# Performance work log

Measured on AMD Instinct MI355X. Metric: run time of the kernel, lower is better.

The kernel has to match this reference:

```python
import jax, jax.numpy as jnp
import numpy as np


def setup_inputs() -> dict:
    key = jax.random.key(0)
    ks = jax.random.split(key, 8)
    dim, E = 128, 8
    b, t, h, w = 2, 16, 64, 64
    scale = 1.0 / np.sqrt(dim)
    return {
        "x": jax.random.normal(ks[0], (b, dim, t, h, w), jnp.float32),
        "gate_w": jax.random.normal(ks[1], (dim, E), jnp.float32) * scale,
        "gate_b": jax.random.normal(ks[2], (E,), jnp.float32) * 0.01,
        "W1": jax.random.normal(ks[3], (E, dim, dim), jnp.float32) * scale,
        "b1": jax.random.normal(ks[4], (E, dim), jnp.float32) * 0.01,
        "alpha": jnp.full((E,), 0.25, jnp.float32),  # PReLU default init
        "W2": jax.random.normal(ks[5], (E, dim, dim), jnp.float32) * scale,
        "b2": jax.random.normal(ks[6], (E, dim), jnp.float32) * 0.01,
        "top_k": 2,
    }


def reference(x, gate_w, gate_b, W1, b1, alpha, W2, b2, top_k):
    b, c, t, h, w = x.shape
    E = gate_w.shape[1]
    # tokens: [N, c] with N = b*t*h*w (matches permute(0,2,3,4,1).reshape(-1,c))
    xf = jnp.transpose(x, (0, 2, 3, 4, 1)).reshape(-1, c)
    N = xf.shape[0]
    logits = xf @ gate_w + gate_b                      # [N, E]
    vals, idx = jax.lax.top_k(logits, top_k)           # [N, K]
    probs = jax.nn.softmax(vals, axis=1)               # softmax over selected logits
    # scatter combine weights to dense [N, E] (zero for unselected experts)
    combine = jnp.zeros((N, E), xf.dtype).at[jnp.arange(N)[:, None], idx].add(probs)
    # expert MLP (1x1x1 conv == per-token linear), scalar PReLU per expert
    h1 = jnp.einsum('nc,eoc->eno', xf, W1) + b1[:, None, :]          # [E, N, c]
    h1 = jnp.maximum(h1, 0) + alpha[:, None, None] * jnp.minimum(h1, 0)
    h2 = jnp.einsum('eno,epo->enp', h1, W2) + b2[:, None, :]         # [E, N, c]
    out = jnp.einsum('ne,enc->nc', combine, h2)                      # weighted combine
    out = jnp.transpose(out.reshape(b, t, h, w, c), (0, 4, 1, 2, 3))
    return out + x
```

## Files before the change

### kernel.cpp

```cpp
#include <hip/hip_runtime.h>

typedef float f32x4 __attribute__((ext_vector_type(4)));
typedef __bf16 bf16x8 __attribute__((ext_vector_type(8)));

#define SPAT 65536
#define CH   128
#define NE   8

#define XS_OFF   0
#define WA_OFF   65536
#define WB_OFF   98304
#define PL_OFF   65536
#define SEL_OFF  131072
#define Q_OFF    132096
#define CB_OFF   134144
#define B1_OFF   138240
#define B2T_OFF  142336
#define AL_OFF   144384
#define LDS_BYTES 144416

static __device__ __forceinline__ unsigned short f2b(float f) {
    unsigned u = __builtin_bit_cast(unsigned, f);
    unsigned r = u + 0x7FFFu + ((u >> 16) & 1u);
    return (unsigned short)(r >> 16);
}
static __device__ __forceinline__ unsigned pk2(float a, float b) {
    return (unsigned)f2b(a) | ((unsigned)f2b(b) << 16);
}

typedef const __attribute__((address_space(1))) void* as1cp;
typedef __attribute__((address_space(3))) void* as3p;
static __device__ __forceinline__ void gload16(const void* g, void* l) {
    __builtin_amdgcn_global_load_lds((as1cp)g, (as3p)l, 16, 0, 0);
}

__global__ void conv_w(const float* __restrict__ W1, const float* __restrict__ W2,
                       unsigned char* __restrict__ wimg) {
    const int gid = blockIdx.x * 256 + threadIdx.x;
    const int mat = gid >> 14;
    const int e   = (gid >> 11) & 7;
    const int o   = (gid >> 4) & 127;
    const int g   = gid & 15;
    const float* s = (mat ? W2 : W1) + (e * 16384 + o * 128 + g * 8);
    uint4 p;
    p.x = pk2(s[0], s[1]); p.y = pk2(s[2], s[3]);
    p.z = pk2(s[4], s[5]); p.w = pk2(s[6], s[7]);
    *(uint4*)(wimg + mat * 262144 + e * 32768 + o * 256 + ((g ^ (o & 7)) * 16)) = p;
}

__global__ __launch_bounds__(1024) __attribute__((amdgpu_waves_per_eu(4, 4)))
void moe_main(const float* __restrict__ x,  const float* __restrict__ gw,
              const float* __restrict__ gb, const float* __restrict__ b1,
              const float* __restrict__ alpha, const float* __restrict__ b2,
              const unsigned char* __restrict__ wimg, float* __restrict__ out)
{
    __shared__ __align__(16) unsigned char smem[LDS_BYTES];
    const int t = threadIdx.x, lane = t & 63, w = t >> 6, blk = blockIdx.x;
    const size_t xbase = (size_t)(blk >> 8) * (size_t)(CH * SPAT) + (size_t)((blk & 255) << 8);

    if (t < 256) ((f32x4*)(smem + B1_OFF))[t] = ((const f32x4*)b1)[t];
    else if (t >= 256 && t < 384) {
        const int j = t - 256;
        uint4 p;
        p.x = pk2(b2[0 * 128 + j], b2[1 * 128 + j]);
        p.y = pk2(b2[2 * 128 + j], b2[3 * 128 + j]);
        p.z = pk2(b2[4 * 128 + j], b2[5 * 128 + j]);
        p.w = pk2(b2[6 * 128 + j], b2[7 * 128 + j]);
        *(uint4*)(smem + B2T_OFF + j * 16) = p;
    } else if (t >= 384 && t < 392) {
        ((float*)(smem + AL_OFF))[t - 384] = alpha[t - 384];
    }

    {
        const int m = t & 255, p = t >> 8;
        f32x4 plo = {0.f,0.f,0.f,0.f}, phi = {0.f,0.f,0.f,0.f};
        #pragma unroll
        for (int cc = 0; cc < 4; ++cc) {
            const int c0 = p * 32 + cc * 8;
            float v[8];
            #pragma unroll
            for (int j = 0; j < 8; ++j) v[j] = x[xbase + (size_t)(c0 + j) * SPAT + m];
            #pragma unroll
            for (int j = 0; j < 8; ++j) {
                const f32x4 g0 = *(const f32x4*)(gw + (c0 + j) * NE);
                const f32x4 g1 = *(const f32x4*)(gw + (c0 + j) * NE + 4);
                plo += v[j] * g0; phi += v[j] * g1;
            }
            uint4 pkv;
            pkv.x = pk2(v[0], v[1]); pkv.y = pk2(v[2], v[3]);
            pkv.z = pk2(v[4], v[5]); pkv.w = pk2(v[6], v[7]);
            const int g = p * 4 + cc;
            *(uint4*)(smem + XS_OFF + m * 256 + ((g ^ (m & 7)) * 16)) = pkv;
        }
        float* pl = (float*)(smem + PL_OFF);
        #pragma unroll
        for (int e2 = 0; e2 < 4; ++e2) {
            pl[(p * 8 + e2)     * 256 + m] = plo[e2];
            pl[(p * 8 + 4 + e2) * 256 + m] = phi[e2];
        }
    }
    __syncthreads();
    if (t < 256) {
        const int m = t;
        const float* pl = (const float*)(smem + PL_OFF);
        float lg[8];
        #pragma unroll
        for (int e2 = 0; e2 < 8; ++e2) lg[e2] = gb[e2];
        #pragma unroll
        for (int pp = 0; pp < 4; ++pp)
            #pragma unroll
            for (int e2 = 0; e2 < 8; ++e2) lg[e2] += pl[(pp * 8 + e2) * 256 + m];
        int i0 = 0; float v0 = lg[0];
        #pragma unroll
        for (int e2 = 1; e2 < 8; ++e2) if (lg[e2] > v0) { v0 = lg[e2]; i0 = e2; }
        int i1 = -1; float v1 = -3.4e38f;
        #pragma unroll
        for (int e2 = 0; e2 < 8; ++e2) if (e2 != i0 && lg[e2] > v1) { v1 = lg[e2]; i1 = e2; }
        const float d  = expf(v1 - v0);
        const float q0 = 1.f / (1.f + d);
        const float q1 = d   / (1.f + d);
        ((unsigned*)(smem + SEL_OFF))[m] = (unsigned)i0 | ((unsigned)i1 << 8);
        ((float*)(smem + Q_OFF))[m * 2]     = q0;
        ((float*)(smem + Q_OFF))[m * 2 + 1] = q1;
        float cb[8];
        #pragma unroll
        for (int e2 = 0; e2 < 8; ++e2) cb[e2] = (e2 == i0) ? q0 : ((e2 == i1) ? q1 : 0.f);
        uint4 cw;
        cw.x = pk2(cb[0], cb[1]); cw.y = pk2(cb[2], cb[3]);
        cw.z = pk2(cb[4], cb[5]); cw.w = pk2(cb[6], cb[7]);
        *(uint4*)(smem + CB_OFF + m * 16) = cw;
    }
    __syncthreads();

    {
        const int goff = w * 1024 + lane * 16, loff = w * 1024;
        #pragma unroll
        for (int r = 0; r < 2; ++r) {
            gload16(wimg + r * 16384 + goff,          smem + WA_OFF + r * 16384 + loff);
            gload16(wimg + 262144 + r * 16384 + goff, smem + WB_OFF + r * 16384 + loff);
        }
    }

    const int mg = w >> 3, ng = w & 7, col = lane & 15, kq = lane >> 4;

    int sel[2]; float cp0[2], cp1[2];
    #pragma unroll
    for (int nf = 0; nf < 2; ++nf) {
        const int tk = ng * 32 + nf * 16 + col;
        sel[nf] = ((const unsigned*)(smem + SEL_OFF))[tk];
        cp0[nf] = ((const float*)(smem + Q_OFF))[tk * 2];
        cp1[nf] = ((const float*)(smem + Q_OFF))[tk * 2 + 1];
    }
    uint4 xb[2][4];
    #pragma unroll
    for (int nf = 0; nf < 2; ++nf) {
        const int row = ng * 32 + nf * 16 + col;
        #pragma unroll
        for (int kt = 0; kt < 4; ++kt)
            xb[nf][kt] = *(const uint4*)(smem + XS_OFF + row * 256 + (((kt * 4 + kq) ^ (row & 7)) * 16));
    }
    __syncthreads();

    f32x4 acc[2][4] = {};

    for (int e = 0; e < NE; ++e) {
        const float alph = ((const float*)(smem + AL_OFF))[e];
        #pragma unroll
        for (int ml = 0; ml < 4; ++ml) {
            const int o = mg * 64 + ml * 16 + col;
            uint4 a1[4];
            #pragma unroll
            for (int kt = 0; kt < 4; ++kt)
                a1[kt] = *(const uint4*)(smem + WA_OFF + o * 256 + (((kt * 4 + kq) ^ (o & 7)) * 16));
            f32x4 h[2] = {};
            #pragma unroll
            for (int kt = 0; kt < 4; ++kt)
                #pragma unroll
                for (int nf = 0; nf < 2; ++nf)
                    h[nf] = __builtin_amdgcn_mfma_f32_16x16x32_bf16(
                        __builtin_bit_cast(bf16x8, a1[kt]),
                        __builtin_bit_cast(bf16x8, xb[nf][kt]), h[nf], 0, 0, 0);
            const int o0 = mg * 64 + ml * 16 + kq * 4;
            const f32x4 b1v = *(const f32x4*)(smem + B1_OFF + e * 512 + o0 * 4);
            #pragma unroll
            for (int nf = 0; nf < 2; ++nf) {
                const float ce = ((sel[nf] & 255) == e) ? cp0[nf]
                               : ((((sel[nf] >> 8) & 255) == e) ? cp1[nf] : 0.f);
                float hv[4];
                #pragma unroll
                for (int i = 0; i < 4; ++i) {
                    float z = h[nf][i] + b1v[i];
                    z = (z > 0.f) ? z : alph * z;
                    hv[i] = z * ce;
                }
                const int tok = ng * 32 + nf * 16 + col;
                const int g   = o0 >> 3;
                uint2 pw; pw.x = pk2(hv[0], hv[1]); pw.y = pk2(hv[2], hv[3]);
                *(uint2*)(smem + XS_OFF + tok * 256 + ((g ^ (tok & 7)) * 16) + ((o0 & 4) << 1)) = pw;
            }
        }
        __syncthreads();
        if (e < 7) {
            const int goff = w * 1024 + lane * 16, loff = w * 1024;
            const unsigned char* src = wimg + (e + 1) * 32768;
            #pragma unroll
            for (int r = 0; r < 2; ++r)
                gload16(src + r * 16384 + goff, smem + WA_OFF + r * 16384 + loff);
        }
        #pragma unroll
        for (int kt = 0; kt < 4; ++kt) {
            uint4 hb[2], wf[4];
            #pragma unroll
            for (int m2 = 0; m2 < 2; ++m2) {
                const int tok = ng * 32 + m2 * 16 + col;
                hb[m2] = *(const uint4*)(smem + XS_OFF + tok * 256 + (((kt * 4 + kq) ^ (tok & 7)) * 16));
            }
            #pragma unroll
            for (int n2 = 0; n2 < 4; ++n2) {
                const int o2 = mg * 64 + n2 * 16 + col;
                wf[n2] = *(const uint4*)(smem + WB_OFF + o2 * 256 + (((kt * 4 + kq) ^ (o2 & 7)) * 16));
            }
            #pragma unroll
            for (int m2 = 0; m2 < 2; ++m2)
                #pragma unroll
                for (int n2 = 0; n2 < 4; ++n2)
                    acc[m2][n2] = __builtin_amdgcn_mfma_f32_16x16x32_bf16(
                        __builtin_bit_cast(bf16x8, hb[m2]),
                        __builtin_bit_cast(bf16x8, wf[n2]), acc[m2][n2], 0, 0, 0);
        }
        __syncthreads();
        if (e < 7) {
            const int goff = w * 1024 + lane * 16, loff = w * 1024;
            const unsigned char* src = wimg + 262144 + (e + 1) * 32768;
            #pragma unroll
            for (int r = 0; r < 2; ++r)
                gload16(src + r * 16384 + goff, smem + WB_OFF + r * 16384 + loff);
        }
    }

    {
        const uint4 z4 = {0u, 0u, 0u, 0u};
        uint4 paf[2], pbf[4];
        #pragma unroll
        for (int m2 = 0; m2 < 2; ++m2) {
            const int tok = ng * 32 + m2 * 16 + col;
            paf[m2] = (kq == 0) ? *(const uint4*)(smem + CB_OFF + tok * 16) : z4;
        }
        #pragma unroll
        for (int n2 = 0; n2 < 4; ++n2) {
            const int o2 = mg * 64 + n2 * 16 + col;
            pbf[n2] = (kq == 0) ? *(const uint4*)(smem + B2T_OFF + o2 * 16) : z4;
        }
        #pragma unroll
        for (int m2 = 0; m2 < 2; ++m2)
            #pragma unroll
            for (int n2 = 0; n2 < 4; ++n2)
                acc[m2][n2] = __builtin_amdgcn_mfma_f32_16x16x32_bf16(
                    __builtin_bit_cast(bf16x8, paf[m2]),
                    __builtin_bit_cast(bf16x8, pbf[n2]), acc[m2][n2], 0, 0, 0);
    }

    #pragma unroll
    for (int m2 = 0; m2 < 2; ++m2) {
        const int tok0 = ng * 32 + m2 * 16 + kq * 4;
        #pragma unroll
        for (int n2 = 0; n2 < 4; ++n2) {
            const int o2 = mg * 64 + n2 * 16 + col;
            const size_t a = xbase + (size_t)o2 * SPAT + tok0;
            const f32x4 xv = *(const f32x4*)(x + a);
            f32x4 r = acc[m2][n2];
            r += xv;
            *(f32x4*)(out + a) = r;
        }
    }
}

extern "C" void kernel_launch(void* const* d_in, const int* in_sizes, int n_in,
                              void* d_out, int out_size, void* d_ws, size_t ws_size,
                              hipStream_t stream) {
    const float* x  = (const float*)d_in[0];
    const float* gw = (const float*)d_in[1];
    const float* gb = (const float*)d_in[2];
    const float* W1 = (const float*)d_in[3];
    const float* b1 = (const float*)d_in[4];
    const float* al = (const float*)d_in[5];
    const float* W2 = (const float*)d_in[6];
    const float* b2 = (const float*)d_in[7];
    (void)in_sizes; (void)n_in; (void)out_size; (void)ws_size;
    unsigned char* wimg = (unsigned char*)d_ws;
    float* out = (float*)d_out;

    conv_w<<<dim3(128), dim3(256), 0, stream>>>(W1, W2, wimg);
    moe_main<<<dim3(512), dim3(1024), 0, stream>>>(x, gw, gb, b1, al, b2, wimg, out);
}
```

Before: 145.0 us.

## Keep expert hidden activations in registers and double-buffer expert weights in LDS

Each wave now owns 16 tokens across all 128 output channels, not a 64x32 tile. The first GEMM's output is packed directly into MFMA A-operand registers for the second GEMM, which works because the W1 rows are permuted at conversion so the accumulator layout matches the needed K ordering. This removes the LDS write/read round trip of the hidden activations. Expert weights now sit in four 32KB LDS slots and are prefetched two experts ahead, replacing the single-buffered reload after each barrier. In exchange, each wave reads the full weight matrices from LDS, increasing LDS read traffic per wave, and register pressure goes up.

```diff
diff --git a/kernel.cpp b/kernel.cpp
--- a/kernel.cpp
+++ b/kernel.cpp
@@ -7,9 +7,8 @@
 #define CH   128
 #define NE   8
 
+#define SLOT(i)  ((i) * 32768)
 #define XS_OFF   0
-#define WA_OFF   65536
-#define WB_OFF   98304
 #define PL_OFF   65536
 #define SEL_OFF  131072
 #define Q_OFF    132096
@@ -41,11 +40,21 @@
     const int e   = (gid >> 11) & 7;
     const int o   = (gid >> 4) & 127;
     const int g   = gid & 15;
-    const float* s = (mat ? W2 : W1) + (e * 16384 + o * 128 + g * 8);
+    int src_row = o;
+    if (mat == 0)
+        src_row = ((o >> 5) << 5) + (((o >> 2) & 3) << 3) + (((o >> 4) & 1) << 2) + (o & 3);
+    const float* s = (mat ? W2 : W1) + (e * 16384 + src_row * 128 + g * 8);
     uint4 p;
     p.x = pk2(s[0], s[1]); p.y = pk2(s[2], s[3]);
     p.z = pk2(s[4], s[5]); p.w = pk2(s[6], s[7]);
     *(uint4*)(wimg + mat * 262144 + e * 32768 + o * 256 + ((g ^ (o & 7)) * 16)) = p;
+}
+
+static __device__ __forceinline__ void stage_w(const unsigned char* __restrict__ src,
+                                               unsigned char* dst, int t) {
+    const int off = t * 16;
+    gload16(src + off,         dst + off);
+    gload16(src + 16384 + off, dst + 16384 + off);
 }
 
 __global__ __launch_bounds__(1024) __attribute__((amdgpu_waves_per_eu(4, 4)))
@@ -57,6 +66,8 @@
     __shared__ __align__(16) unsigned char smem[LDS_BYTES];
     const int t = threadIdx.x, lane = t & 63, w = t >> 6, blk = blockIdx.x;
     const size_t xbase = (size_t)(blk >> 8) * (size_t)(CH * SPAT) + (size_t)((blk & 255) << 8);
+
+    stage_w(wimg, smem + SLOT(3), t);
 
     if (t < 256) ((f32x4*)(smem + B1_OFF))[t] = ((const f32x4*)b1)[t];
     else if (t >= 256 && t < 384) {
@@ -132,146 +143,99 @@
     }
     __syncthreads();
 
-    {
-        const int goff = w * 1024 + lane * 16, loff = w * 1024;
-        #pragma unroll
-        for (int r = 0; r < 2; ++r) {
-            gload16(wimg + r * 16384 + goff,          smem + WA_OFF + r * 16384 + loff);
-            gload16(wimg + 262144 + r * 16384 + goff, smem + WB_OFF + r * 16384 + loff);
-        }
-    }
-
-    const int mg = w >> 3, ng = w & 7, col = lane & 15, kq = lane >> 4;
-
-    int sel[2]; float cp0[2], cp1[2];
+    const int col = lane & 15, kq = lane >> 4;
+    const int tokA = w * 16 + col;
+    const unsigned selu = ((const unsigned*)(smem + SEL_OFF))[tokA];
+    const float cq0 = ((const float*)(smem + Q_OFF))[tokA * 2];
+    const float cq1 = ((const float*)(smem + Q_OFF))[tokA * 2 + 1];
+
+    uint4 xb[4];
     #pragma unroll
-    for (int nf = 0; nf < 2; ++nf) {
-        const int tk = ng * 32 + nf * 16 + col;
-        sel[nf] = ((const unsigned*)(smem + SEL_OFF))[tk];
-        cp0[nf] = ((const float*)(smem + Q_OFF))[tk * 2];
-        cp1[nf] = ((const float*)(smem + Q_OFF))[tk * 2 + 1];
-    }
-    uint4 xb[2][4];
-    #pragma unroll
-    for (int nf = 0; nf < 2; ++nf) {
-        const int row = ng * 32 + nf * 16 + col;
-        #pragma unroll
-        for (int kt = 0; kt < 4; ++kt)
-            xb[nf][kt] = *(const uint4*)(smem + XS_OFF + row * 256 + (((kt * 4 + kq) ^ (row & 7)) * 16));
-    }
+    for (int kt = 0; kt < 4; ++kt)
+        xb[kt] = *(const uint4*)(smem + XS_OFF + tokA * 256 + (((kt * 4 + kq) ^ (tokA & 7)) * 16));
     __syncthreads();
 
-    f32x4 acc[2][4] = {};
-
+    stage_w(wimg + 262144,         smem + SLOT(0), t);
+    stage_w(wimg + 32768,          smem + SLOT(1), t);
+    stage_w(wimg + 262144 + 32768, smem + SLOT(2), t);
+
+    f32x4 acc[8] = {};
+
+    #pragma unroll 1
     for (int e = 0; e < NE; ++e) {
+        const unsigned waOff = 0x18000u ^ ((unsigned)(e & 1) << 16);
+        const unsigned wbOff = ((unsigned)(e & 1) << 16);
+        const unsigned char* WA = smem + waOff;
+        const unsigned char* WB = smem + wbOff;
         const float alph = ((const float*)(smem + AL_OFF))[e];
-        #pragma unroll
-        for (int ml = 0; ml < 4; ++ml) {
-            const int o = mg * 64 + ml * 16 + col;
+        const float ce = ((selu & 255u) == (unsigned)e) ? cq0
+                       : ((((selu >> 8) & 255u) == (unsigned)e) ? cq1 : 0.f);
+
+        uint4 pa[4];
+        #pragma unroll
+        for (int ml = 0; ml < 8; ++ml) {
+            const int o = ml * 16 + col;
             uint4 a1[4];
             #pragma unroll
             for (int kt = 0; kt < 4; ++kt)
-                a1[kt] = *(const uint4*)(smem + WA_OFF + o * 256 + (((kt * 4 + kq) ^ (o & 7)) * 16));
-            f32x4 h[2] = {};
+                a1[kt] = *(const uint4*)(WA + o * 256 + (((kt * 4 + kq) ^ (o & 7)) * 16));
+            f32x4 h = {0.f, 0.f, 0.f, 0.f};
             #pragma unroll
             for (int kt = 0; kt < 4; ++kt)
-                #pragma unroll
-                for (int nf = 0; nf < 2; ++nf)
-                    h[nf] = __builtin_amdgcn_mfma_f32_16x16x32_bf16(
+                h = __builtin_amdgcn_mfma_f32_16x16x32_bf16(
                         __builtin_bit_cast(bf16x8, a1[kt]),
-                        __builtin_bit_cast(bf16x8, xb[nf][kt]), h[nf], 0, 0, 0);
-            const int o0 = mg * 64 + ml * 16 + kq * 4;
-            const f32x4 b1v = *(const f32x4*)(smem + B1_OFF + e * 512 + o0 * 4);
-            #pragma unroll
-            for (int nf = 0; nf < 2; ++nf) {
-                const float ce = ((sel[nf] & 255) == e) ? cp0[nf]
-                               : ((((sel[nf] >> 8) & 255) == e) ? cp1[nf] : 0.f);
-                float hv[4];
-                #pragma unroll
-                for (int i = 0; i < 4; ++i) {
-                    float z = h[nf][i] + b1v[i];
-                    z = (z > 0.f) ? z : alph * z;
-                    hv[i] = z * ce;
-                }
-                const int tok = ng * 32 + nf * 16 + col;
-                const int g   = o0 >> 3;
-                uint2 pw; pw.x = pk2(hv[0], hv[1]); pw.y = pk2(hv[2], hv[3]);
-                *(uint2*)(smem + XS_OFF + tok * 256 + ((g ^ (tok & 7)) * 16) + ((o0 & 4) << 1)) = pw;
+                        __builtin_bit_cast(bf16x8, xb[kt]), h, 0, 0, 0);
+            const int ob = ((ml >> 1) << 5) + (kq << 3) + ((ml & 1) << 2);
+            const f32x4 b1v = *(const f32x4*)(smem + B1_OFF + e * 512 + ob * 4);
+            float hv[4];
+            #pragma unroll
+            for (int i = 0; i < 4; ++i) {
+                float z = h[i] + b1v[i];
+                z = (z > 0.f) ? z : alph * z;
+                hv[i] = z * ce;
             }
+            ((unsigned*)&pa[ml >> 1])[(ml & 1) * 2]     = pk2(hv[0], hv[1]);
+            ((unsigned*)&pa[ml >> 1])[(ml & 1) * 2 + 1] = pk2(hv[2], hv[3]);
         }
         __syncthreads();
-        if (e < 7) {
-            const int goff = w * 1024 + lane * 16, loff = w * 1024;
-            const unsigned char* src = wimg + (e + 1) * 32768;
-            #pragma unroll
-            for (int r = 0; r < 2; ++r)
-                gload16(src + r * 16384 + goff, smem + WA_OFF + r * 16384 + loff);
-        }
+        if (e < 6) stage_w(wimg + (e + 2) * 32768, smem + waOff, t);
+
         #pragma unroll
         for (int kt = 0; kt < 4; ++kt) {
-            uint4 hb[2], wf[4];
-            #pragma unroll
-            for (int m2 = 0; m2 < 2; ++m2) {
-                const int tok = ng * 32 + m2 * 16 + col;
-                hb[m2] = *(const uint4*)(smem + XS_OFF + tok * 256 + (((kt * 4 + kq) ^ (tok & 7)) * 16));
+            #pragma unroll
+            for (int n2 = 0; n2 < 8; ++n2) {
+                const int o2 = n2 * 16 + col;
+                const uint4 wf = *(const uint4*)(WB + o2 * 256 + (((kt * 4 + kq) ^ (o2 & 7)) * 16));
+                acc[n2] = __builtin_amdgcn_mfma_f32_16x16x32_bf16(
+                        __builtin_bit_cast(bf16x8, pa[kt]),
+                        __builtin_bit_cast(bf16x8, wf), acc[n2], 0, 0, 0);
             }
-            #pragma unroll
-            for (int n2 = 0; n2 < 4; ++n2) {
-                const int o2 = mg * 64 + n2 * 16 + col;
-                wf[n2] = *(const uint4*)(smem + WB_OFF + o2 * 256 + (((kt * 4 + kq) ^ (o2 & 7)) * 16));
-            }
-            #pragma unroll
-            for (int m2 = 0; m2 < 2; ++m2)
-                #pragma unroll
-                for (int n2 = 0; n2 < 4; ++n2)
-                    acc[m2][n2] = __builtin_amdgcn_mfma_f32_16x16x32_bf16(
-                        __builtin_bit_cast(bf16x8, hb[m2]),
-                        __builtin_bit_cast(bf16x8, wf[n2]), acc[m2][n2], 0, 0, 0);
         }
         __syncthreads();
-        if (e < 7) {
-            const int goff = w * 1024 + lane * 16, loff = w * 1024;
-            const unsigned char* src = wimg + 262144 + (e + 1) * 32768;
-            #pragma unroll
-            for (int r = 0; r < 2; ++r)
-                gload16(src + r * 16384 + goff, smem + WB_OFF + r * 16384 + loff);
-        }
+        if (e < 6) stage_w(wimg + 262144 + (e + 2) * 32768, smem + wbOff, t);
     }
 
     {
         const uint4 z4 = {0u, 0u, 0u, 0u};
-        uint4 paf[2], pbf[4];
-        #pragma unroll
-        for (int m2 = 0; m2 < 2; ++m2) {
-            const int tok = ng * 32 + m2 * 16 + col;
-            paf[m2] = (kq == 0) ? *(const uint4*)(smem + CB_OFF + tok * 16) : z4;
-        }
-        #pragma unroll
-        for (int n2 = 0; n2 < 4; ++n2) {
-            const int o2 = mg * 64 + n2 * 16 + col;
-            pbf[n2] = (kq == 0) ? *(const uint4*)(smem + B2T_OFF + o2 * 16) : z4;
-        }
-        #pragma unroll
-        for (int m2 = 0; m2 < 2; ++m2)
-            #pragma unroll
-            for (int n2 = 0; n2 < 4; ++n2)
-                acc[m2][n2] = __builtin_amdgcn_mfma_f32_16x16x32_bf16(
-                    __builtin_bit_cast(bf16x8, paf[m2]),
-                    __builtin_bit_cast(bf16x8, pbf[n2]), acc[m2][n2], 0, 0, 0);
-    }
-
+        const uint4 paf = (kq == 0) ? *(const uint4*)(smem + CB_OFF + tokA * 16) : z4;
+        #pragma unroll
+        for (int n2 = 0; n2 < 8; ++n2) {
+            const uint4 pbf = (kq == 0) ? *(const uint4*)(smem + B2T_OFF + (n2 * 16 + col) * 16) : z4;
+            acc[n2] = __builtin_amdgcn_mfma_f32_16x16x32_bf16(
+                    __builtin_bit_cast(bf16x8, paf),
+                    __builtin_bit_cast(bf16x8, pbf), acc[n2], 0, 0, 0);
+        }
+    }
+
+    const int tok0 = w * 16 + kq * 4;
     #pragma unroll
-    for (int m2 = 0; m2 < 2; ++m2) {
-        const int tok0 = ng * 32 + m2 * 16 + kq * 4;
-        #pragma unroll
-        for (int n2 = 0; n2 < 4; ++n2) {
-            const int o2 = mg * 64 + n2 * 16 + col;
-            const size_t a = xbase + (size_t)o2 * SPAT + tok0;
-            const f32x4 xv = *(const f32x4*)(x + a);
-            f32x4 r = acc[m2][n2];
-            r += xv;
-            *(f32x4*)(out + a) = r;
-        }
+    for (int n2 = 0; n2 < 8; ++n2) {
+        const int o2 = n2 * 16 + col;
+        const size_t a = xbase + (size_t)o2 * SPAT + tok0;
+        const f32x4 xv = *(const f32x4*)(x + a);
+        f32x4 r = acc[n2];
+        r += xv;
+        *(f32x4*)(out + a) = r;
     }
 }
 
```

After: 154.4 us. +6.5%, slower.
